# Performance work log

Measured on AMD Instinct MI355X. Metric: run time of the kernel, lower is better.

## Reference

```python
import jax, jax.numpy as jnp
import numpy as np

SCALE = 2.0 / 0.24  # UniformBoxWarp(sidelength=0.24)

def pos_embed(x, max_logscale, n_freqs):
    freqs = 2.0 ** jnp.linspace(0.0, float(max_logscale), n_freqs).astype(x.dtype)
    xb = x[..., None, :] * freqs[:, None]                  # (b, n, F, 3)
    sc = jnp.stack([jnp.sin(xb), jnp.cos(xb)], axis=-2)    # (b, n, F, 2, 3)
    sc = sc.reshape(x.shape[:-1] + (n_freqs * 2 * 3,))
    return jnp.concatenate([x, sc], axis=-1)

def film(x, W, b, freq, phase):
    # x: (b, n, in); freq/phase: (b, out) broadcast over points
    h = jnp.einsum('bni,oi->bno', x, W) + b
    return jnp.sin(freq[:, None, :] * h + phase[:, None, :])

def split_style(style):
    # rearrange 'b (2 d) -> b d 2'; freq = first half * 15 + 30, phase = second half
    d = style.shape[-1] // 2
    return style[:, :d] * 15.0 + 30.0, style[:, d:]

def setup_inputs() -> dict:
    key = jax.random.key(0)
    ks = jax.random.split(key, 14)
    B, N, H = 4, 65536, 256
    dim_pos, dim_dir = 63, 27
    r = lambda k, shp, s=1.0: jax.random.normal(k, shp, dtype=jnp.float32) * s
    return {
        'input': r(ks[0], (B, N, 3)),
        'ray_directions': r(ks[1], (B, N, 3)),
        'style_network': r(ks[2], (B, 4 * H)),
        'style_color': r(ks[3], (B, 2 * H)),
        'W1': r(ks[4], (H, dim_pos), 1.0 / dim_pos),
        'b1': jnp.zeros((H,), jnp.float32),
        'W2': r(ks[5], (H, H), np.sqrt(6.0 / H) / 25.0),
        'b2': jnp.zeros((H,), jnp.float32),
        'Wf': r(ks[6], (1, H), np.sqrt(6.0 / H) / 25.0),
        'bf': jnp.zeros((1,), jnp.float32),
        'Wcs': r(ks[7], (H, H + dim_dir), np.sqrt(6.0 / (H + dim_dir)) / 25.0),
        'bcs': jnp.zeros((H,), jnp.float32),
        'Wcl': r(ks[8], (3, H), np.sqrt(6.0 / H) / 25.0),
        'bcl': jnp.zeros((3,), jnp.float32),
    }

def reference(input, ray_directions, style_network, style_color,
              W1, b1, W2, b2, Wf, bf, Wcs, bcs, Wcl, bcl):
    H = W1.shape[0]
    pe = pos_embed(input * SCALE, 9, 10)                 # (b, n, 63)
    fn, pn = split_style(style_network)                  # (b, 2H) each
    x = film(pe, W1, b1, fn[:, :H], pn[:, :H])
    x = film(x, W2, b2, fn[:, H:], pn[:, H:])
    sigma = jnp.einsum('bnh,oh->bno', x, Wf) + bf        # (b, n, 1)
    de = pos_embed(ray_directions, 3, 4)                 # (b, n, 27)
    fc, pc = split_style(style_color)
    hc = film(jnp.concatenate([de, x], axis=-1), Wcs, bcs, fc, pc)
    rgb = jnp.einsum('bnh,oh->bno', hc, Wcl) + bcl       # (b, n, 3)
    return jnp.concatenate([rgb, sigma], axis=-1)        # (b, n, 4)
```

## Files before the change

kernel.cpp:

```cpp
#include <hip/hip_runtime.h>


#define SCALE_F 8.333333333333334f

typedef _Float16 hf;
typedef __attribute__((ext_vector_type(8)))  _Float16 hf8;
typedef __attribute__((ext_vector_type(16))) float f32x16;

__device__ __forceinline__ float redrev(float x) {
  const float chi = 0.15915494309189535f;
  const float clo = 6.4206383e-09f;
  float n = rintf(x * chi);
  float d = __builtin_fmaf(x, chi, -n);
  return __builtin_fmaf(x, clo, d);
}
__device__ __forceinline__ float fsin(float x) { return __builtin_amdgcn_sinf(redrev(x)); }
__device__ __forceinline__ float fcos(float x) { return __builtin_amdgcn_cosf(redrev(x)); }
__device__ __forceinline__ float sinrev(float t) { return __builtin_amdgcn_sinf(t - rintf(t)); }

#define INV2PI 0.15915494309189535f
#define C15R   2.3873241463784303f
#define C30R   4.7746482927568605f

__device__ __forceinline__ unsigned pk2h(hf a, hf b) {
  return ((unsigned)__builtin_bit_cast(unsigned short, a)) |
         (((unsigned)__builtin_bit_cast(unsigned short, b)) << 16);
}

__global__ void prep_w(const float* __restrict__ W1, const float* __restrict__ W2,
                       const float* __restrict__ Wcs, unsigned short* __restrict__ wsu)
{
  int t = blockIdx.x * 256 + threadIdx.x;
  if (t >= 155648) return;
  int L, pos, base;
  if (t < 16384)      { L = 0; pos = t;         base = 0; }
  else if (t < 81920) { L = 1; pos = t - 16384; base = 32768; }
  else                { L = 2; pos = t - 81920; base = 163840; }
  int kstep = pos >> 12, r = pos & 4095;
  int ot = (r >> 9) & 7, kh = (r >> 8) & 1, o5 = (r >> 3) & 31, j = r & 7;
  int o = ot * 32 + o5, k = kstep * 16 + kh * 8 + j;
  float wv = 0.f;
  if (L == 0)      { if (k < 63) wv = W1[o * 63 + k]; }
  else if (L == 1) { wv = W2[o * 256 + k]; }
  else { if (k < 256) wv = Wcs[o * 283 + 27 + k];
         else { int q = k - 256; if (q < 27) wv = Wcs[o * 283 + q]; } }
  hf hh = (hf)wv;
  hf ll = (hf)((wv - (float)hh) * 1024.0f);
  wsu[base + kstep * 8192 + r]        = __builtin_bit_cast(unsigned short, hh);
  wsu[base + kstep * 8192 + 4096 + r] = __builtin_bit_cast(unsigned short, ll);
}

__device__ __forceinline__ float peval(float x0, float x1, float x2, int k) {
  if (k >= 63) return 0.f;
  if (k < 3) return (k == 0) ? x0 : ((k == 1) ? x1 : x2);
  int rr = k - 3, f = rr / 6, rem = rr - f * 6;
  int d = (rem < 3) ? rem : rem - 3;
  float xa = (d == 0) ? x0 : ((d == 1) ? x1 : x2);
  float arg = xa * (float)(1 << f);
  return (rem < 3) ? fsin(arg) : fcos(arg);
}
__device__ __forceinline__ float deval(float r0, float r1, float r2, int k) {
  if (k >= 27) return 0.f;
  if (k < 3) return (k == 0) ? r0 : ((k == 1) ? r1 : r2);
  int rr = k - 3, f = rr / 6, rem = rr - f * 6;
  int d = (rem < 3) ? rem : rem - 3;
  float ra = (d == 0) ? r0 : ((d == 1) ? r1 : r2);
  float arg = ra * (float)(1 << f);
  return (rem < 3) ? fsin(arg) : fcos(arg);
}
__device__ __forceinline__ void build_de(float r0, float r1, float r2, int kbase,
                                         hf8& hh, hf8& ll) {
  unsigned uh[4], ul[4];
  #pragma unroll
  for (int jj = 0; jj < 4; ++jj) {
    float va = deval(r0, r1, r2, kbase + 2 * jj), vb = deval(r0, r1, r2, kbase + 2 * jj + 1);
    hf ha = (hf)va, hb = (hf)vb;
    uh[jj] = pk2h(ha, hb);
    ul[jj] = pk2h((hf)((va - (float)ha) * 1024.f), (hf)((vb - (float)hb) * 1024.f));
  }
  uint4 vh = make_uint4(uh[0], uh[1], uh[2], uh[3]);
  uint4 vl = make_uint4(ul[0], ul[1], ul[2], ul[3]);
  hh = __builtin_bit_cast(hf8, vh);
  ll = __builtin_bit_cast(hf8, vl);
}

__device__ __forceinline__ void stage_slab(const unsigned short* __restrict__ prep, int ks,
                                           unsigned short* lWb, int wv, int lane) {
  const char* src = (const char*)prep + (size_t)ks * 16384 + wv * 2048 + lane * 16;
  char* dst = (char*)lWb + wv * 2048;
  __builtin_amdgcn_global_load_lds((const unsigned int*)src, (unsigned int*)dst, 16, 0, 0);
  __builtin_amdgcn_global_load_lds((const unsigned int*)(src + 1024),
                                   (unsigned int*)(dst + 1024), 16, 0, 0);
}

__device__ __forceinline__ void kstep_mfma(const unsigned short* lwb, int wbA,
                                           hf8 Bh0, hf8 Bh1, hf8 Bl0, hf8 Bl1,
                                           f32x16& a00, f32x16& a01,
                                           f32x16& a10, f32x16& a11) {
  const hf sc = (hf)0.0009765625f;
  hf8 Bh0s = Bh0 * sc, Bh1s = Bh1 * sc, Bl0s = Bl0 * sc, Bl1s = Bl1 * sc;
  hf8 Ah0 = *(const hf8*)&lwb[wbA];
  hf8 Al0 = *(const hf8*)&lwb[4096 + wbA];
  hf8 Ah1 = *(const hf8*)&lwb[wbA + 512];
  hf8 Al1 = *(const hf8*)&lwb[4096 + wbA + 512];
  a00 = __builtin_amdgcn_mfma_f32_32x32x16_f16(Ah0, Bh0,  a00, 0, 0, 0);
  a00 = __builtin_amdgcn_mfma_f32_32x32x16_f16(Al0, Bh0s, a00, 0, 0, 0);
  a00 = __builtin_amdgcn_mfma_f32_32x32x16_f16(Ah0, Bl0s, a00, 0, 0, 0);
  a01 = __builtin_amdgcn_mfma_f32_32x32x16_f16(Ah0, Bh1,  a01, 0, 0, 0);
  a01 = __builtin_amdgcn_mfma_f32_32x32x16_f16(Al0, Bh1s, a01, 0, 0, 0);
  a01 = __builtin_amdgcn_mfma_f32_32x32x16_f16(Ah0, Bl1s, a01, 0, 0, 0);
  a10 = __builtin_amdgcn_mfma_f32_32x32x16_f16(Ah1, Bh0,  a10, 0, 0, 0);
  a10 = __builtin_amdgcn_mfma_f32_32x32x16_f16(Al1, Bh0s, a10, 0, 0, 0);
  a10 = __builtin_amdgcn_mfma_f32_32x32x16_f16(Ah1, Bl0s, a10, 0, 0, 0);
  a11 = __builtin_amdgcn_mfma_f32_32x32x16_f16(Ah1, Bh1,  a11, 0, 0, 0);
  a11 = __builtin_amdgcn_mfma_f32_32x32x16_f16(Al1, Bh1s, a11, 0, 0, 0);
  a11 = __builtin_amdgcn_mfma_f32_32x32x16_f16(Ah1, Bl1s, a11, 0, 0, 0);
}

template <int NKTOT, int NLX>
__device__ __forceinline__ void layer_loop(
    const unsigned short* __restrict__ prep, unsigned short* lW,
    const unsigned short* lX, int ptA, int ptB, int h, int wbA, int wv, int lane,
    f32x16& a00, f32x16& a01, f32x16& a10, f32x16& a11,
    hf8 dhA0, hf8 dhB0, hf8 dhA1, hf8 dhB1,
    hf8 dlA0, hf8 dlB0, hf8 dlA1, hf8 dlB1)
{
  stage_slab(prep, 0, lW, wv, lane);
  if (NKTOT > 1) stage_slab(prep, 1, lW + 8192, wv, lane);
  const int bA = ptA * 256, bB = ptB * 256, sA = ptA & 7, sB = ptB & 7;
  #pragma unroll 1
  for (int ks = 0; ks < NLX; ++ks) {
    if (ks + 1 < NKTOT) asm volatile("s_waitcnt vmcnt(2)" ::: "memory");
    else                asm volatile("s_waitcnt vmcnt(0)" ::: "memory");
    __syncthreads();
    int slot = ks * 2 + h;
    hf8 Bh0 = *(const hf8*)&lX[bA + ((slot ^ sA) << 3)];
    hf8 Bh1 = *(const hf8*)&lX[bB + ((slot ^ sB) << 3)];
    hf8 Bl0 = *(const hf8*)&lX[32768 + bA + ((slot ^ sA) << 3)];
    hf8 Bl1 = *(const hf8*)&lX[32768 + bB + ((slot ^ sB) << 3)];
    kstep_mfma(lW + (ks & 1) * 8192, wbA, Bh0, Bh1, Bl0, Bl1, a00, a01, a10, a11);
    __syncthreads();
    if (ks + 2 < NKTOT) stage_slab(prep, ks + 2, lW + (ks & 1) * 8192, wv, lane);
  }
  if (NLX < NKTOT) {
    asm volatile("s_waitcnt vmcnt(2)" ::: "memory");
    __syncthreads();
    kstep_mfma(lW + (NLX & 1) * 8192, wbA, dhA0, dhB0, dlA0, dlB0, a00, a01, a10, a11);
    __syncthreads();
    asm volatile("s_waitcnt vmcnt(0)" ::: "memory");
    __syncthreads();
    kstep_mfma(lW + ((NLX + 1) & 1) * 8192, wbA, dhA1, dhB1, dlA1, dlB1, a00, a01, a10, a11);
    __syncthreads();
  }
}

__device__ __forceinline__ void store_pair(unsigned short* lX, int pt, int slot, int off,
                                           float v0, float v1, float v2, float v3)
{
  hf h0 = (hf)v0, h1 = (hf)v1, h2 = (hf)v2, h3 = (hf)v3;
  int base = pt * 256 + ((slot ^ (pt & 7)) << 3) + off;
  *(uint2*)&lX[base] = make_uint2(pk2h(h0, h1), pk2h(h2, h3));
  hf r0 = (hf)((v0 - (float)h0) * 1024.f), r1 = (hf)((v1 - (float)h1) * 1024.f);
  hf r2 = (hf)((v2 - (float)h2) * 1024.f), r3 = (hf)((v3 - (float)h3) * 1024.f);
  *(uint2*)&lX[32768 + base] = make_uint2(pk2h(r0, r1), pk2h(r2, r3));
}

__global__ void __launch_bounds__(512, 1)
siren_mfma(const float* __restrict__ input, const float* __restrict__ rdir,
           const float* __restrict__ sn, const float* __restrict__ sc,
           const float* __restrict__ b1, const float* __restrict__ b2,
           const float* __restrict__ Wf, const float* __restrict__ bfp,
           const float* __restrict__ bcs, const float* __restrict__ Wcl,
           const float* __restrict__ bcl, const unsigned short* __restrict__ wsu,
           float* __restrict__ out)
{
  __shared__ __align__(16) unsigned char smem[163840];
  unsigned short* lX = (unsigned short*)smem;
  unsigned short* lW = (unsigned short*)(smem + 131072);
  float* lP = (float*)smem;

  const int tid = threadIdx.x;
  const int w = tid >> 6, lane = tid & 63;
  const int ow = w >> 1, pw = w & 1;
  const int l31 = lane & 31, h = lane >> 5;
  const int gpt0 = blockIdx.x << 7;
  const int b = blockIdx.x >> 9;
  const int ptA = pw * 64 + l31, ptB = ptA + 32;
  const int wbA = ow * 1024 + h * 256 + l31 * 8;
  const float* snb = sn + b * 1024;
  const float* scb = sc + b * 512;

  float rA0, rA1, rA2, rB0, rB1, rB2;
  {
    const float* rp = rdir + (size_t)(gpt0 + ptA) * 3;
    rA0 = rp[0]; rA1 = rp[1]; rA2 = rp[2];
    const float* rq = rdir + (size_t)(gpt0 + ptB) * 3;
    rB0 = rq[0]; rB1 = rq[1]; rB2 = rq[2];
  }

  {
    const int ept = tid & 127, eseg = tid >> 7;
    const float* ip = input + (size_t)(gpt0 + ept) * 3;
    float x0 = ip[0] * SCALE_F, x1 = ip[1] * SCALE_F, x2 = ip[2] * SCALE_F;
    #pragma unroll
    for (int j = 0; j < 4; ++j) {
      int k0 = eseg * 16 + 4 * j;
      float v0 = peval(x0, x1, x2, k0),     v1 = peval(x0, x1, x2, k0 + 1);
      float v2 = peval(x0, x1, x2, k0 + 2), v3 = peval(x0, x1, x2, k0 + 3);
      int slot = eseg * 2 + (j >> 1);
      store_pair(lX, ept, slot, (j & 1) * 4, v0, v1, v2, v3);
    }
  }

  f32x16 a00, a01, a10, a11;
  hf8 hz = {};
  float sp0 = 0.f, sp1 = 0.f;

  #pragma unroll
  for (int oi = 0; oi < 2; ++oi)
    #pragma unroll
    for (int q = 0; q < 4; ++q) {
      int o0 = ow * 64 + oi * 32 + q * 8 + h * 4;
      float4 bv = *(const float4*)&b1[o0];
      f32x16& aA = oi ? a10 : a00; f32x16& aB = oi ? a11 : a01;
      aA[q*4+0] = bv.x; aA[q*4+1] = bv.y; aA[q*4+2] = bv.z; aA[q*4+3] = bv.w;
      aB[q*4+0] = bv.x; aB[q*4+1] = bv.y; aB[q*4+2] = bv.z; aB[q*4+3] = bv.w;
    }
  layer_loop<4, 4>(wsu, lW, lX, ptA, ptB, h, wbA, w, lane, a00, a01, a10, a11,
                   hz, hz, hz, hz, hz, hz, hz, hz);
  #pragma unroll
  for (int oi = 0; oi < 2; ++oi)
    #pragma unroll
    for (int q = 0; q < 4; ++q) {
      int o0 = ow * 64 + oi * 32 + q * 8 + h * 4;
      float4 f4 = *(const float4*)&snb[o0];
      float4 p4 = *(const float4*)&snb[512 + o0];
      float fr0 = __builtin_fmaf(f4.x, C15R, C30R), fr1 = __builtin_fmaf(f4.y, C15R, C30R);
      float fr2 = __builtin_fmaf(f4.z, C15R, C30R), fr3 = __builtin_fmaf(f4.w, C15R, C30R);
      float pr0 = p4.x * INV2PI, pr1 = p4.y * INV2PI, pr2 = p4.z * INV2PI, pr3 = p4.w * INV2PI;
      int slot = ow * 8 + oi * 4 + q;
      #pragma unroll
      for (int pi = 0; pi < 2; ++pi) {
        const f32x16& a = pi ? (oi ? a11 : a01) : (oi ? a10 : a00);
        float v0 = sinrev(__builtin_fmaf(fr0, a[q*4+0], pr0));
        float v1 = sinrev(__builtin_fmaf(fr1, a[q*4+1], pr1));
        float v2 = sinrev(__builtin_fmaf(fr2, a[q*4+2], pr2));
        float v3 = sinrev(__builtin_fmaf(fr3, a[q*4+3], pr3));
        store_pair(lX, pi ? ptB : ptA, slot, h * 4, v0, v1, v2, v3);
      }
    }

  #pragma unroll
  for (int oi = 0; oi < 2; ++oi)
    #pragma unroll
    for (int q = 0; q < 4; ++q) {
      int o0 = ow * 64 + oi * 32 + q * 8 + h * 4;
      float4 bv = *(const float4*)&b2[o0];
      f32x16& aA = oi ? a10 : a00; f32x16& aB = oi ? a11 : a01;
      aA[q*4+0] = bv.x; aA[q*4+1] = bv.y; aA[q*4+2] = bv.z; aA[q*4+3] = bv.w;
      aB[q*4+0] = bv.x; aB[q*4+1] = bv.y; aB[q*4+2] = bv.z; aB[q*4+3] = bv.w;
    }
  layer_loop<16, 16>(wsu + 32768, lW, lX, ptA, ptB, h, wbA, w, lane, a00, a01, a10, a11,
                     hz, hz, hz, hz, hz, hz, hz, hz);
  #pragma unroll
  for (int oi = 0; oi < 2; ++oi)
    #pragma unroll
    for (int q = 0; q < 4; ++q) {
      int o0 = ow * 64 + oi * 32 + q * 8 + h * 4;
      float4 f4 = *(const float4*)&snb[256 + o0];
      float4 p4 = *(const float4*)&snb[768 + o0];
      float4 wf = *(const float4*)&Wf[o0];
      float fr0 = __builtin_fmaf(f4.x, C15R, C30R), fr1 = __builtin_fmaf(f4.y, C15R, C30R);
      float fr2 = __builtin_fmaf(f4.z, C15R, C30R), fr3 = __builtin_fmaf(f4.w, C15R, C30R);
      float pr0 = p4.x * INV2PI, pr1 = p4.y * INV2PI, pr2 = p4.z * INV2PI, pr3 = p4.w * INV2PI;
      int slot = ow * 8 + oi * 4 + q;
      #pragma unroll
      for (int pi = 0; pi < 2; ++pi) {
        const f32x16& a = pi ? (oi ? a11 : a01) : (oi ? a10 : a00);
        float v0 = sinrev(__builtin_fmaf(fr0, a[q*4+0], pr0));
        float v1 = sinrev(__builtin_fmaf(fr1, a[q*4+1], pr1));
        float v2 = sinrev(__builtin_fmaf(fr2, a[q*4+2], pr2));
        float v3 = sinrev(__builtin_fmaf(fr3, a[q*4+3], pr3));
        float s = __builtin_fmaf(wf.x, v0, __builtin_fmaf(wf.y, v1,
                  __builtin_fmaf(wf.z, v2, wf.w * v3)));
        if (pi == 0) sp0 += s; else sp1 += s;
        store_pair(lX, pi ? ptB : ptA, slot, h * 4, v0, v1, v2, v3);
      }
    }

  hf8 dhA0, dhB0, dhA1, dhB1, dlA0, dlB0, dlA1, dlB1;
  build_de(rA0, rA1, rA2, 0 * 16 + h * 8, dhA0, dlA0);
  build_de(rB0, rB1, rB2, 0 * 16 + h * 8, dhB0, dlB0);
  build_de(rA0, rA1, rA2, 1 * 16 + h * 8, dhA1, dlA1);
  build_de(rB0, rB1, rB2, 1 * 16 + h * 8, dhB1, dlB1);

  #pragma unroll
  for (int oi = 0; oi < 2; ++oi)
    #pragma unroll
    for (int q = 0; q < 4; ++q) {
      int o0 = ow * 64 + oi * 32 + q * 8 + h * 4;
      float4 bv = *(const float4*)&bcs[o0];
      f32x16& aA = oi ? a10 : a00; f32x16& aB = oi ? a11 : a01;
      aA[q*4+0] = bv.x; aA[q*4+1] = bv.y; aA[q*4+2] = bv.z; aA[q*4+3] = bv.w;
      aB[q*4+0] = bv.x; aB[q*4+1] = bv.y; aB[q*4+2] = bv.z; aB[q*4+3] = bv.w;
    }
  layer_loop<18, 16>(wsu + 163840, lW, lX, ptA, ptB, h, wbA, w, lane, a00, a01, a10, a11,
                     dhA0, dhB0, dhA1, dhB1, dlA0, dlB0, dlA1, dlB1);
  float q00 = 0.f, q01 = 0.f, q02 = 0.f, q10 = 0.f, q11 = 0.f, q12 = 0.f;
  #pragma unroll
  for (int oi = 0; oi < 2; ++oi)
    #pragma unroll
    for (int q = 0; q < 4; ++q) {
      int o0 = ow * 64 + oi * 32 + q * 8 + h * 4;
      float4 f4 = *(const float4*)&scb[o0];
      float4 p4 = *(const float4*)&scb[256 + o0];
      float4 w0 = *(const float4*)&Wcl[o0];
      float4 w1 = *(const float4*)&Wcl[256 + o0];
      float4 w2 = *(const float4*)&Wcl[512 + o0];
      float fr0 = __builtin_fmaf(f4.x, C15R, C30R), fr1 = __builtin_fmaf(f4.y, C15R, C30R);
      float fr2 = __builtin_fmaf(f4.z, C15R, C30R), fr3 = __builtin_fmaf(f4.w, C15R, C30R);
      float pr0 = p4.x * INV2PI, pr1 = p4.y * INV2PI, pr2 = p4.z * INV2PI, pr3 = p4.w * INV2PI;
      #pragma unroll
      for (int pi = 0; pi < 2; ++pi) {
        const f32x16& a = pi ? (oi ? a11 : a01) : (oi ? a10 : a00);
        float v0 = sinrev(__builtin_fmaf(fr0, a[q*4+0], pr0));
        float v1 = sinrev(__builtin_fmaf(fr1, a[q*4+1], pr1));
        float v2 = sinrev(__builtin_fmaf(fr2, a[q*4+2], pr2));
        float v3 = sinrev(__builtin_fmaf(fr3, a[q*4+3], pr3));
        float t0 = __builtin_fmaf(w0.x, v0, __builtin_fmaf(w0.y, v1, __builtin_fmaf(w0.z, v2, w0.w * v3)));
        float t1 = __builtin_fmaf(w1.x, v0, __builtin_fmaf(w1.y, v1, __builtin_fmaf(w1.z, v2, w1.w * v3)));
        float t2 = __builtin_fmaf(w2.x, v0, __builtin_fmaf(w2.y, v1, __builtin_fmaf(w2.z, v2, w2.w * v3)));
        if (pi == 0) { q00 += t0; q01 += t1; q02 += t2; }
        else         { q10 += t0; q11 += t1; q12 += t2; }
      }
    }

  q00 += __shfl_xor(q00, 32); q01 += __shfl_xor(q01, 32); q02 += __shfl_xor(q02, 32);
  q10 += __shfl_xor(q10, 32); q11 += __shfl_xor(q11, 32); q12 += __shfl_xor(q12, 32);
  sp0 += __shfl_xor(sp0, 32); sp1 += __shfl_xor(sp1, 32);
  if (h == 0) {
    *(float4*)&lP[((w * 2 + 0) * 32 + l31) * 4] = make_float4(q00, q01, q02, sp0);
    *(float4*)&lP[((w * 2 + 1) * 32 + l31) * 4] = make_float4(q10, q11, q12, sp1);
  }
  __syncthreads();

  {
    int ptL = tid >> 2, ch = tid & 3;
    int pwt = ptL >> 6, pit = (ptL >> 5) & 1, lt = ptL & 31;
    float v = 0.f;
    #pragma unroll
    for (int owt = 0; owt < 4; ++owt) {
      int wv_ = (owt * 2 + pwt);
      v += lP[((wv_ * 2 + pit) * 32 + lt) * 4 + ch];
    }
    v += (ch == 3) ? bfp[0] : bcl[ch];
    out[((size_t)gpt0 + ptL) * 4 + ch] = v;
  }
}

extern "C" void kernel_launch(void* const* d_in, const int* in_sizes, int n_in,
                              void* d_out, int out_size, void* d_ws, size_t ws_size,
                              hipStream_t stream) {
  const float* input = (const float*)d_in[0];
  const float* rdir  = (const float*)d_in[1];
  const float* sn    = (const float*)d_in[2];
  const float* sc    = (const float*)d_in[3];
  const float* W1    = (const float*)d_in[4];
  const float* b1    = (const float*)d_in[5];
  const float* W2    = (const float*)d_in[6];
  const float* b2    = (const float*)d_in[7];
  const float* Wf    = (const float*)d_in[8];
  const float* bf    = (const float*)d_in[9];
  const float* Wcs   = (const float*)d_in[10];
  const float* bcs   = (const float*)d_in[11];
  const float* Wcl   = (const float*)d_in[12];
  const float* bcl   = (const float*)d_in[13];
  unsigned short* wsu = (unsigned short*)d_ws;
  float* out = (float*)d_out;

  prep_w<<<608, 256, 0, stream>>>(W1, W2, Wcs, wsu);
  siren_mfma<<<2048, 512, 0, stream>>>(input, rdir, sn, sc, b1, b2, Wf, bf,
                                       bcs, Wcl, bcl, wsu, out);
}
```

Baseline: 320.8 us.

## Halve points per block, store activation residuals as FP8 to shrink LDS

Each block now handles 64 points instead of 128 and keeps one pair of accumulators per wave. The low-order residual of the split-fp16 activations is stored in LDS as scaled FP8 rather than fp16, which cuts shared memory from 160KB to 80KB and allows more resident blocks (launch bounds raised to 4). Weight slab staging is issued early, before the epilogue math of the previous layer, so it overlaps with that work. The cost is extra FP8 decode per k-step, the same weight slab traffic spread over twice as many points, and a less accurate residual term.

```diff
diff --git a/kernel.cpp b/kernel.cpp
--- a/kernel.cpp
+++ b/kernel.cpp
@@ -4,6 +4,8 @@
 #define SCALE_F 8.333333333333334f
 
 typedef _Float16 hf;
+typedef __attribute__((ext_vector_type(2)))  float f32x2;
+typedef __attribute__((ext_vector_type(2)))  _Float16 hf2;
 typedef __attribute__((ext_vector_type(8)))  _Float16 hf8;
 typedef __attribute__((ext_vector_type(16))) float f32x16;
 
@@ -25,6 +27,25 @@
 __device__ __forceinline__ unsigned pk2h(hf a, hf b) {
   return ((unsigned)__builtin_bit_cast(unsigned short, a)) |
          (((unsigned)__builtin_bit_cast(unsigned short, b)) << 16);
+}
+__device__ __forceinline__ unsigned enc4_fp8(float r0, float r1, float r2, float r3) {
+  int e = __builtin_amdgcn_cvt_pk_fp8_f32(r0, r1, 0, false);
+  e = __builtin_amdgcn_cvt_pk_fp8_f32(r2, r3, e, true);
+  return (unsigned)e;
+}
+__device__ __forceinline__ hf8 dec8_fp8(uint2 enc) {
+  const float dsc = 0.015625f;
+  f32x2 f0 = __builtin_amdgcn_cvt_pk_f32_fp8((int)enc.x, false);
+  f32x2 f1 = __builtin_amdgcn_cvt_pk_f32_fp8((int)enc.x, true);
+  f32x2 f2 = __builtin_amdgcn_cvt_pk_f32_fp8((int)enc.y, false);
+  f32x2 f3 = __builtin_amdgcn_cvt_pk_f32_fp8((int)enc.y, true);
+  hf2 h0 = __builtin_bit_cast(hf2, __builtin_amdgcn_cvt_pkrtz(f0.x * dsc, f0.y * dsc));
+  hf2 h1 = __builtin_bit_cast(hf2, __builtin_amdgcn_cvt_pkrtz(f1.x * dsc, f1.y * dsc));
+  hf2 h2 = __builtin_bit_cast(hf2, __builtin_amdgcn_cvt_pkrtz(f2.x * dsc, f2.y * dsc));
+  hf2 h3 = __builtin_bit_cast(hf2, __builtin_amdgcn_cvt_pkrtz(f3.x * dsc, f3.y * dsc));
+  uint4 u = make_uint4(__builtin_bit_cast(unsigned, h0), __builtin_bit_cast(unsigned, h1),
+                       __builtin_bit_cast(unsigned, h2), __builtin_bit_cast(unsigned, h3));
+  return __builtin_bit_cast(hf8, u);
 }
 
 __global__ void prep_w(const float* __restrict__ W1, const float* __restrict__ W2,
@@ -76,7 +97,7 @@
     float va = deval(r0, r1, r2, kbase + 2 * jj), vb = deval(r0, r1, r2, kbase + 2 * jj + 1);
     hf ha = (hf)va, hb = (hf)vb;
     uh[jj] = pk2h(ha, hb);
-    ul[jj] = pk2h((hf)((va - (float)ha) * 1024.f), (hf)((vb - (float)hb) * 1024.f));
+    ul[jj] = pk2h((hf)(va - (float)ha), (hf)(vb - (float)hb));
   }
   uint4 vh = make_uint4(uh[0], uh[1], uh[2], uh[3]);
   uint4 vl = make_uint4(ul[0], ul[1], ul[2], ul[3]);
@@ -92,80 +113,75 @@
   __builtin_amdgcn_global_load_lds((const unsigned int*)(src + 1024),
                                    (unsigned int*)(dst + 1024), 16, 0, 0);
 }
+__device__ __forceinline__ void stage2(const unsigned short* __restrict__ prep,
+                                       unsigned short* lW, int wv, int lane) {
+  stage_slab(prep, 0, lW, wv, lane);
+  stage_slab(prep, 1, lW + 8192, wv, lane);
+}
 
 __device__ __forceinline__ void kstep_mfma(const unsigned short* lwb, int wbA,
-                                           hf8 Bh0, hf8 Bh1, hf8 Bl0, hf8 Bl1,
-                                           f32x16& a00, f32x16& a01,
-                                           f32x16& a10, f32x16& a11) {
+                                           hf8 Bh, hf8 Blv, f32x16& a0, f32x16& a1) {
   const hf sc = (hf)0.0009765625f;
-  hf8 Bh0s = Bh0 * sc, Bh1s = Bh1 * sc, Bl0s = Bl0 * sc, Bl1s = Bl1 * sc;
+  hf8 Bhs = Bh * sc;
   hf8 Ah0 = *(const hf8*)&lwb[wbA];
   hf8 Al0 = *(const hf8*)&lwb[4096 + wbA];
   hf8 Ah1 = *(const hf8*)&lwb[wbA + 512];
   hf8 Al1 = *(const hf8*)&lwb[4096 + wbA + 512];
-  a00 = __builtin_amdgcn_mfma_f32_32x32x16_f16(Ah0, Bh0,  a00, 0, 0, 0);
-  a00 = __builtin_amdgcn_mfma_f32_32x32x16_f16(Al0, Bh0s, a00, 0, 0, 0);
-  a00 = __builtin_amdgcn_mfma_f32_32x32x16_f16(Ah0, Bl0s, a00, 0, 0, 0);
-  a01 = __builtin_amdgcn_mfma_f32_32x32x16_f16(Ah0, Bh1,  a01, 0, 0, 0);
-  a01 = __builtin_amdgcn_mfma_f32_32x32x16_f16(Al0, Bh1s, a01, 0, 0, 0);
-  a01 = __builtin_amdgcn_mfma_f32_32x32x16_f16(Ah0, Bl1s, a01, 0, 0, 0);
-  a10 = __builtin_amdgcn_mfma_f32_32x32x16_f16(Ah1, Bh0,  a10, 0, 0, 0);
-  a10 = __builtin_amdgcn_mfma_f32_32x32x16_f16(Al1, Bh0s, a10, 0, 0, 0);
-  a10 = __builtin_amdgcn_mfma_f32_32x32x16_f16(Ah1, Bl0s, a10, 0, 0, 0);
-  a11 = __builtin_amdgcn_mfma_f32_32x32x16_f16(Ah1, Bh1,  a11, 0, 0, 0);
-  a11 = __builtin_amdgcn_mfma_f32_32x32x16_f16(Al1, Bh1s, a11, 0, 0, 0);
-  a11 = __builtin_amdgcn_mfma_f32_32x32x16_f16(Ah1, Bl1s, a11, 0, 0, 0);
-}
-
-template <int NKTOT, int NLX>
+  a0 = __builtin_amdgcn_mfma_f32_32x32x16_f16(Ah0, Bh,  a0, 0, 0, 0);
+  a0 = __builtin_amdgcn_mfma_f32_32x32x16_f16(Al0, Bhs, a0, 0, 0, 0);
+  a0 = __builtin_amdgcn_mfma_f32_32x32x16_f16(Ah0, Blv, a0, 0, 0, 0);
+  a1 = __builtin_amdgcn_mfma_f32_32x32x16_f16(Ah1, Bh,  a1, 0, 0, 0);
+  a1 = __builtin_amdgcn_mfma_f32_32x32x16_f16(Al1, Bhs, a1, 0, 0, 0);
+  a1 = __builtin_amdgcn_mfma_f32_32x32x16_f16(Ah1, Blv, a1, 0, 0, 0);
+}
+
+template <int NK, bool DE>
 __device__ __forceinline__ void layer_loop(
     const unsigned short* __restrict__ prep, unsigned short* lW,
-    const unsigned short* lX, int ptA, int ptB, int h, int wbA, int wv, int lane,
-    f32x16& a00, f32x16& a01, f32x16& a10, f32x16& a11,
-    hf8 dhA0, hf8 dhB0, hf8 dhA1, hf8 dhB1,
-    hf8 dlA0, hf8 dlB0, hf8 dlA1, hf8 dlB1)
+    const unsigned short* lXh, const unsigned char* lXl,
+    int pt, int h, int wbA, int wv, int lane,
+    f32x16& a0, f32x16& a1, hf8 dh0, hf8 dh1, hf8 dl0, hf8 dl1)
 {
-  stage_slab(prep, 0, lW, wv, lane);
-  if (NKTOT > 1) stage_slab(prep, 1, lW + 8192, wv, lane);
-  const int bA = ptA * 256, bB = ptB * 256, sA = ptA & 7, sB = ptB & 7;
+  const int NLX = DE ? NK - 2 : NK;
+  const int bh = pt * 256, p7 = pt & 7, p15 = pt & 15;
   #pragma unroll 1
   for (int ks = 0; ks < NLX; ++ks) {
-    if (ks + 1 < NKTOT) asm volatile("s_waitcnt vmcnt(2)" ::: "memory");
-    else                asm volatile("s_waitcnt vmcnt(0)" ::: "memory");
+    if (ks + 1 < NK) asm volatile("s_waitcnt vmcnt(2)" ::: "memory");
+    else             asm volatile("s_waitcnt vmcnt(0)" ::: "memory");
     __syncthreads();
     int slot = ks * 2 + h;
-    hf8 Bh0 = *(const hf8*)&lX[bA + ((slot ^ sA) << 3)];
-    hf8 Bh1 = *(const hf8*)&lX[bB + ((slot ^ sB) << 3)];
-    hf8 Bl0 = *(const hf8*)&lX[32768 + bA + ((slot ^ sA) << 3)];
-    hf8 Bl1 = *(const hf8*)&lX[32768 + bB + ((slot ^ sB) << 3)];
-    kstep_mfma(lW + (ks & 1) * 8192, wbA, Bh0, Bh1, Bl0, Bl1, a00, a01, a10, a11);
-    __syncthreads();
-    if (ks + 2 < NKTOT) stage_slab(prep, ks + 2, lW + (ks & 1) * 8192, wv, lane);
-  }
-  if (NLX < NKTOT) {
+    hf8 Bh = *(const hf8*)&lXh[bh + ((slot ^ p7) << 3)];
+    uint2 enc = *(const uint2*)&lXl[bh + ((slot ^ p15) << 3)];
+    hf8 Blv = dec8_fp8(enc);
+    kstep_mfma(lW + (ks & 1) * 8192, wbA, Bh, Blv, a0, a1);
+    __syncthreads();
+    if (ks + 2 < NK) stage_slab(prep, ks + 2, lW + (ks & 1) * 8192, wv, lane);
+  }
+  if (DE) {
     asm volatile("s_waitcnt vmcnt(2)" ::: "memory");
     __syncthreads();
-    kstep_mfma(lW + (NLX & 1) * 8192, wbA, dhA0, dhB0, dlA0, dlB0, a00, a01, a10, a11);
+    kstep_mfma(lW + (NLX & 1) * 8192, wbA, dh0, dl0, a0, a1);
     __syncthreads();
     asm volatile("s_waitcnt vmcnt(0)" ::: "memory");
     __syncthreads();
-    kstep_mfma(lW + ((NLX + 1) & 1) * 8192, wbA, dhA1, dhB1, dlA1, dlB1, a00, a01, a10, a11);
-    __syncthreads();
-  }
-}
-
-__device__ __forceinline__ void store_pair(unsigned short* lX, int pt, int slot, int off,
-                                           float v0, float v1, float v2, float v3)
+    kstep_mfma(lW + ((NLX + 1) & 1) * 8192, wbA, dh1, dl1, a0, a1);
+    __syncthreads();
+  }
+}
+
+__device__ __forceinline__ void store4(unsigned short* lXh, unsigned char* lXl,
+                                       int pt, int slot, int h,
+                                       float v0, float v1, float v2, float v3)
 {
   hf h0 = (hf)v0, h1 = (hf)v1, h2 = (hf)v2, h3 = (hf)v3;
-  int base = pt * 256 + ((slot ^ (pt & 7)) << 3) + off;
-  *(uint2*)&lX[base] = make_uint2(pk2h(h0, h1), pk2h(h2, h3));
-  hf r0 = (hf)((v0 - (float)h0) * 1024.f), r1 = (hf)((v1 - (float)h1) * 1024.f);
-  hf r2 = (hf)((v2 - (float)h2) * 1024.f), r3 = (hf)((v3 - (float)h3) * 1024.f);
-  *(uint2*)&lX[32768 + base] = make_uint2(pk2h(r0, r1), pk2h(r2, r3));
-}
-
-__global__ void __launch_bounds__(512, 1)
+  *(uint2*)&lXh[pt * 256 + ((slot ^ (pt & 7)) << 3) + h * 4] =
+      make_uint2(pk2h(h0, h1), pk2h(h2, h3));
+  *(unsigned*)&lXl[pt * 256 + ((slot ^ (pt & 15)) << 3) + h * 4] =
+      enc4_fp8((v0 - (float)h0) * 64.f, (v1 - (float)h1) * 64.f,
+               (v2 - (float)h2) * 64.f, (v3 - (float)h3) * 64.f);
+}
+
+__global__ void __launch_bounds__(512, 4)
 siren_mfma(const float* __restrict__ input, const float* __restrict__ rdir,
            const float* __restrict__ sn, const float* __restrict__ sc,
            const float* __restrict__ b1, const float* __restrict__ b2,
@@ -174,47 +190,52 @@
            const float* __restrict__ bcl, const unsigned short* __restrict__ wsu,
            float* __restrict__ out)
 {
-  __shared__ __align__(16) unsigned char smem[163840];
-  unsigned short* lX = (unsigned short*)smem;
-  unsigned short* lW = (unsigned short*)(smem + 131072);
+  __shared__ __align__(16) unsigned char smem[81920];
+  unsigned short* lXh = (unsigned short*)smem;
+  unsigned char*  lXl = smem + 32768;
+  unsigned short* lW  = (unsigned short*)(smem + 49152);
   float* lP = (float*)smem;
 
   const int tid = threadIdx.x;
   const int w = tid >> 6, lane = tid & 63;
   const int ow = w >> 1, pw = w & 1;
   const int l31 = lane & 31, h = lane >> 5;
-  const int gpt0 = blockIdx.x << 7;
-  const int b = blockIdx.x >> 9;
-  const int ptA = pw * 64 + l31, ptB = ptA + 32;
+  const int gpt0 = blockIdx.x << 6;
+  const int b = blockIdx.x >> 10;
+  const int pt = pw * 32 + l31;
   const int wbA = ow * 1024 + h * 256 + l31 * 8;
   const float* snb = sn + b * 1024;
   const float* scb = sc + b * 512;
 
-  float rA0, rA1, rA2, rB0, rB1, rB2;
+  stage2(wsu, lW, w, lane);
+
+  float rA0, rA1, rA2;
   {
-    const float* rp = rdir + (size_t)(gpt0 + ptA) * 3;
+    const float* rp = rdir + (size_t)(gpt0 + pt) * 3;
     rA0 = rp[0]; rA1 = rp[1]; rA2 = rp[2];
-    const float* rq = rdir + (size_t)(gpt0 + ptB) * 3;
-    rB0 = rq[0]; rB1 = rq[1]; rB2 = rq[2];
   }
 
   {
-    const int ept = tid & 127, eseg = tid >> 7;
+    const int ept = tid & 63, seg = tid >> 6;
     const float* ip = input + (size_t)(gpt0 + ept) * 3;
     float x0 = ip[0] * SCALE_F, x1 = ip[1] * SCALE_F, x2 = ip[2] * SCALE_F;
-    #pragma unroll
-    for (int j = 0; j < 4; ++j) {
-      int k0 = eseg * 16 + 4 * j;
-      float v0 = peval(x0, x1, x2, k0),     v1 = peval(x0, x1, x2, k0 + 1);
-      float v2 = peval(x0, x1, x2, k0 + 2), v3 = peval(x0, x1, x2, k0 + 3);
-      int slot = eseg * 2 + (j >> 1);
-      store_pair(lX, ept, slot, (j & 1) * 4, v0, v1, v2, v3);
-    }
-  }
-
-  f32x16 a00, a01, a10, a11;
+    float vv[8];
+    #pragma unroll
+    for (int jj = 0; jj < 8; ++jj) vv[jj] = peval(x0, x1, x2, seg * 8 + jj);
+    hf c0=(hf)vv[0], c1=(hf)vv[1], c2=(hf)vv[2], c3=(hf)vv[3];
+    hf c4=(hf)vv[4], c5=(hf)vv[5], c6=(hf)vv[6], c7=(hf)vv[7];
+    *(uint4*)&lXh[ept * 256 + ((seg ^ (ept & 7)) << 3)] =
+        make_uint4(pk2h(c0,c1), pk2h(c2,c3), pk2h(c4,c5), pk2h(c6,c7));
+    *(uint2*)&lXl[ept * 256 + ((seg ^ (ept & 15)) << 3)] = make_uint2(
+        enc4_fp8((vv[0]-(float)c0)*64.f, (vv[1]-(float)c1)*64.f,
+                 (vv[2]-(float)c2)*64.f, (vv[3]-(float)c3)*64.f),
+        enc4_fp8((vv[4]-(float)c4)*64.f, (vv[5]-(float)c5)*64.f,
+                 (vv[6]-(float)c6)*64.f, (vv[7]-(float)c7)*64.f));
+  }
+
+  f32x16 a0, a1;
   hf8 hz = {};
-  float sp0 = 0.f, sp1 = 0.f;
+  float sp = 0.f;
 
   #pragma unroll
   for (int oi = 0; oi < 2; ++oi)
@@ -222,12 +243,11 @@
     for (int q = 0; q < 4; ++q) {
       int o0 = ow * 64 + oi * 32 + q * 8 + h * 4;
       float4 bv = *(const float4*)&b1[o0];
-      f32x16& aA = oi ? a10 : a00; f32x16& aB = oi ? a11 : a01;
-      aA[q*4+0] = bv.x; aA[q*4+1] = bv.y; aA[q*4+2] = bv.z; aA[q*4+3] = bv.w;
-      aB[q*4+0] = bv.x; aB[q*4+1] = bv.y; aB[q*4+2] = bv.z; aB[q*4+3] = bv.w;
-    }
-  layer_loop<4, 4>(wsu, lW, lX, ptA, ptB, h, wbA, w, lane, a00, a01, a10, a11,
-                   hz, hz, hz, hz, hz, hz, hz, hz);
+      f32x16& a = oi ? a1 : a0;
+      a[q*4+0] = bv.x; a[q*4+1] = bv.y; a[q*4+2] = bv.z; a[q*4+3] = bv.w;
+    }
+  layer_loop<4, false>(wsu, lW, lXh, lXl, pt, h, wbA, w, lane, a0, a1, hz, hz, hz, hz);
+  stage2(wsu + 32768, lW, w, lane);
   #pragma unroll
   for (int oi = 0; oi < 2; ++oi)
     #pragma unroll
@@ -235,19 +255,12 @@
       int o0 = ow * 64 + oi * 32 + q * 8 + h * 4;
       float4 f4 = *(const float4*)&snb[o0];
       float4 p4 = *(const float4*)&snb[512 + o0];
-      float fr0 = __builtin_fmaf(f4.x, C15R, C30R), fr1 = __builtin_fmaf(f4.y, C15R, C30R);
-      float fr2 = __builtin_fmaf(f4.z, C15R, C30R), fr3 = __builtin_fmaf(f4.w, C15R, C30R);
-      float pr0 = p4.x * INV2PI, pr1 = p4.y * INV2PI, pr2 = p4.z * INV2PI, pr3 = p4.w * INV2PI;
-      int slot = ow * 8 + oi * 4 + q;
-      #pragma unroll
-      for (int pi = 0; pi < 2; ++pi) {
-        const f32x16& a = pi ? (oi ? a11 : a01) : (oi ? a10 : a00);
-        float v0 = sinrev(__builtin_fmaf(fr0, a[q*4+0], pr0));
-        float v1 = sinrev(__builtin_fmaf(fr1, a[q*4+1], pr1));
-        float v2 = sinrev(__builtin_fmaf(fr2, a[q*4+2], pr2));
-        float v3 = sinrev(__builtin_fmaf(fr3, a[q*4+3], pr3));
-        store_pair(lX, pi ? ptB : ptA, slot, h * 4, v0, v1, v2, v3);
-      }
+      const f32x16& a = oi ? a1 : a0;
+      float v0 = sinrev(__builtin_fmaf(__builtin_fmaf(f4.x, C15R, C30R), a[q*4+0], p4.x * INV2PI));
+      float v1 = sinrev(__builtin_fmaf(__builtin_fmaf(f4.y, C15R, C30R), a[q*4+1], p4.y * INV2PI));
+      float v2 = sinrev(__builtin_fmaf(__builtin_fmaf(f4.z, C15R, C30R), a[q*4+2], p4.z * INV2PI));
+      float v3 = sinrev(__builtin_fmaf(__builtin_fmaf(f4.w, C15R, C30R), a[q*4+3], p4.w * INV2PI));
+      store4(lXh, lXl, pt, ow * 8 + oi * 4 + q, h, v0, v1, v2, v3);
     }
 
   #pragma unroll
@@ -256,12 +269,11 @@
     for (int q = 0; q < 4; ++q) {
       int o0 = ow * 64 + oi * 32 + q * 8 + h * 4;
       float4 bv = *(const float4*)&b2[o0];
-      f32x16& aA = oi ? a10 : a00; f32x16& aB = oi ? a11 : a01;
-      aA[q*4+0] = bv.x; aA[q*4+1] = bv.y; aA[q*4+2] = bv.z; aA[q*4+3] = bv.w;
-      aB[q*4+0] = bv.x; aB[q*4+1] = bv.y; aB[q*4+2] = bv.z; aB[q*4+3] = bv.w;
-    }
-  layer_loop<16, 16>(wsu + 32768, lW, lX, ptA, ptB, h, wbA, w, lane, a00, a01, a10, a11,
-                     hz, hz, hz, hz, hz, hz, hz, hz);
+      f32x16& a = oi ? a1 : a0;
+      a[q*4+0] = bv.x; a[q*4+1] = bv.y; a[q*4+2] = bv.z; a[q*4+3] = bv.w;
+    }
+  layer_loop<16, false>(wsu + 32768, lW, lXh, lXl, pt, h, wbA, w, lane, a0, a1, hz, hz, hz, hz);
+  stage2(wsu + 163840, lW, w, lane);
   #pragma unroll
   for (int oi = 0; oi < 2; ++oi)
     #pragma unroll
@@ -270,29 +282,19 @@
       float4 f4 = *(const float4*)&snb[256 + o0];
       float4 p4 = *(const float4*)&snb[768 + o0];
       float4 wf = *(const float4*)&Wf[o0];
-      float fr0 = __builtin_fmaf(f4.x, C15R, C30R), fr1 = __builtin_fmaf(f4.y, C15R, C30R);
-      float fr2 = __builtin_fmaf(f4.z, C15R, C30R), fr3 = __builtin_fmaf(f4.w, C15R, C30R);
-      float pr0 = p4.x * INV2PI, pr1 = p4.y * INV2PI, pr2 = p4.z * INV2PI, pr3 = p4.w * INV2PI;
-      int slot = ow * 8 + oi * 4 + q;
-      #pragma unroll
-      for (int pi = 0; pi < 2; ++pi) {
-        const f32x16& a = pi ? (oi ? a11 : a01) : (oi ? a10 : a00);
-        float v0 = sinrev(__builtin_fmaf(fr0, a[q*4+0], pr0));
-        float v1 = sinrev(__builtin_fmaf(fr1, a[q*4+1], pr1));
-        float v2 = sinrev(__builtin_fmaf(fr2, a[q*4+2], pr2));
-        float v3 = sinrev(__builtin_fmaf(fr3, a[q*4+3], pr3));
-        float s = __builtin_fmaf(wf.x, v0, __builtin_fmaf(wf.y, v1,
-                  __builtin_fmaf(wf.z, v2, wf.w * v3)));
-        if (pi == 0) sp0 += s; else sp1 += s;
-        store_pair(lX, pi ? ptB : ptA, slot, h * 4, v0, v1, v2, v3);
-      }
-    }
-
-  hf8 dhA0, dhB0, dhA1, dhB1, dlA0, dlB0, dlA1, dlB1;
-  build_de(rA0, rA1, rA2, 0 * 16 + h * 8, dhA0, dlA0);
-  build_de(rB0, rB1, rB2, 0 * 16 + h * 8, dhB0, dlB0);
-  build_de(rA0, rA1, rA2, 1 * 16 + h * 8, dhA1, dlA1);
-  build_de(rB0, rB1, rB2, 1 * 16 + h * 8, dhB1, dlB1);
+      const f32x16& a = oi ? a1 : a0;
+      float v0 = sinrev(__builtin_fmaf(__builtin_fmaf(f4.x, C15R, C30R), a[q*4+0], p4.x * INV2PI));
+      float v1 = sinrev(__builtin_fmaf(__builtin_fmaf(f4.y, C15R, C30R), a[q*4+1], p4.y * INV2PI));
+      float v2 = sinrev(__builtin_fmaf(__builtin_fmaf(f4.z, C15R, C30R), a[q*4+2], p4.z * INV2PI));
+      float v3 = sinrev(__builtin_fmaf(__builtin_fmaf(f4.w, C15R, C30R), a[q*4+3], p4.w * INV2PI));
+      sp = __builtin_fmaf(wf.x, v0, __builtin_fmaf(wf.y, v1,
+           __builtin_fmaf(wf.z, v2, __builtin_fmaf(wf.w, v3, sp))));
+      store4(lXh, lXl, pt, ow * 8 + oi * 4 + q, h, v0, v1, v2, v3);
+    }
+
+  hf8 dh0, dh1, dl0, dl1;
+  build_de(rA0, rA1, rA2, 0 * 16 + h * 8, dh0, dl0);
+  build_de(rA0, rA1, rA2, 1 * 16 + h * 8, dh1, dl1);
 
   #pragma unroll
   for (int oi = 0; oi < 2; ++oi)
@@ -300,13 +302,12 @@
     for (int q = 0; q < 4; ++q) {
       int o0 = ow * 64 + oi * 32 + q * 8 + h * 4;
       float4 bv = *(const float4*)&bcs[o0];
-      f32x16& aA = oi ? a10 : a00; f32x16& aB = oi ? a11 : a01;
-      aA[q*4+0] = bv.x; aA[q*4+1] = bv.y; aA[q*4+2] = bv.z; aA[q*4+3] = bv.w;
-      aB[q*4+0] = bv.x; aB[q*4+1] = bv.y; aB[q*4+2] = bv.z; aB[q*4+3] = bv.w;
-    }
-  layer_loop<18, 16>(wsu + 163840, lW, lX, ptA, ptB, h, wbA, w, lane, a00, a01, a10, a11,
-                     dhA0, dhB0, dhA1, dhB1, dlA0, dlB0, dlA1, dlB1);
-  float q00 = 0.f, q01 = 0.f, q02 = 0.f, q10 = 0.f, q11 = 0.f, q12 = 0.f;
+      f32x16& a = oi ? a1 : a0;
+      a[q*4+0] = bv.x; a[q*4+1] = bv.y; a[q*4+2] = bv.z; a[q*4+3] = bv.w;
+    }
+  layer_loop<18, true>(wsu + 163840, lW, lXh, lXl, pt, h, wbA, w, lane, a0, a1,
+                       dh0, dh1, dl0, dl1);
+  float q0 = 0.f, q1 = 0.f, q2 = 0.f;
   #pragma unroll
   for (int oi = 0; oi < 2; ++oi)
     #pragma unroll
@@ -317,42 +318,29 @@
       float4 w0 = *(const float4*)&Wcl[o0];
       float4 w1 = *(const float4*)&Wcl[256 + o0];
       float4 w2 = *(const float4*)&Wcl[512 + o0];
-      float fr0 = __builtin_fmaf(f4.x, C15R, C30R), fr1 = __builtin_fmaf(f4.y, C15R, C30R);
-      float fr2 = __builtin_fmaf(f4.z, C15R, C30R), fr3 = __builtin_fmaf(f4.w, C15R, C30R);
-      float pr0 = p4.x * INV2PI, pr1 = p4.y * INV2PI, pr2 = p4.z * INV2PI, pr3 = p4.w * INV2PI;
-      #pragma unroll
-      for (int pi = 0; pi < 2; ++pi) {
-        const f32x16& a = pi ? (oi ? a11 : a01) : (oi ? a10 : a00);
-        float v0 = sinrev(__builtin_fmaf(fr0, a[q*4+0], pr0));
-        float v1 = sinrev(__builtin_fmaf(fr1, a[q*4+1], pr1));
-        float v2 = sinrev(__builtin_fmaf(fr2, a[q*4+2], pr2));
-        float v3 = sinrev(__builtin_fmaf(fr3, a[q*4+3], pr3));
-        float t0 = __builtin_fmaf(w0.x, v0, __builtin_fmaf(w0.y, v1, __builtin_fmaf(w0.z, v2, w0.w * v3)));
-        float t1 = __builtin_fmaf(w1.x, v0, __builtin_fmaf(w1.y, v1, __builtin_fmaf(w1.z, v2, w1.w * v3)));
-        float t2 = __builtin_fmaf(w2.x, v0, __builtin_fmaf(w2.y, v1, __builtin_fmaf(w2.z, v2, w2.w * v3)));
-        if (pi == 0) { q00 += t0; q01 += t1; q02 += t2; }
-        else         { q10 += t0; q11 += t1; q12 += t2; }
-      }
-    }
-
-  q00 += __shfl_xor(q00, 32); q01 += __shfl_xor(q01, 32); q02 += __shfl_xor(q02, 32);
-  q10 += __shfl_xor(q10, 32); q11 += __shfl_xor(q11, 32); q12 += __shfl_xor(q12, 32);
-  sp0 += __shfl_xor(sp0, 32); sp1 += __shfl_xor(sp1, 32);
-  if (h == 0) {
-    *(float4*)&lP[((w * 2 + 0) * 32 + l31) * 4] = make_float4(q00, q01, q02, sp0);
-    *(float4*)&lP[((w * 2 + 1) * 32 + l31) * 4] = make_float4(q10, q11, q12, sp1);
-  }
+      const f32x16& a = oi ? a1 : a0;
+      float v0 = sinrev(__builtin_fmaf(__builtin_fmaf(f4.x, C15R, C30R), a[q*4+0], p4.x * INV2PI));
+      float v1 = sinrev(__builtin_fmaf(__builtin_fmaf(f4.y, C15R, C30R), a[q*4+1], p4.y * INV2PI));
+      float v2 = sinrev(__builtin_fmaf(__builtin_fmaf(f4.z, C15R, C30R), a[q*4+2], p4.z * INV2PI));
+      float v3 = sinrev(__builtin_fmaf(__builtin_fmaf(f4.w, C15R, C30R), a[q*4+3], p4.w * INV2PI));
+      q0 = __builtin_fmaf(w0.x, v0, __builtin_fmaf(w0.y, v1, __builtin_fmaf(w0.z, v2, __builtin_fmaf(w0.w, v3, q0))));
+      q1 = __builtin_fmaf(w1.x, v0, __builtin_fmaf(w1.y, v1, __builtin_fmaf(w1.z, v2, __builtin_fmaf(w1.w, v3, q1))));
+      q2 = __builtin_fmaf(w2.x, v0, __builtin_fmaf(w2.y, v1, __builtin_fmaf(w2.z, v2, __builtin_fmaf(w2.w, v3, q2))));
+    }
+
+  q0 += __shfl_xor(q0, 32); q1 += __shfl_xor(q1, 32); q2 += __shfl_xor(q2, 32);
+  sp += __shfl_xor(sp, 32);
+  if (h == 0)
+    *(float4*)&lP[(w * 32 + l31) * 4] = make_float4(q0, q1, q2, sp);
   __syncthreads();
 
-  {
+  if (tid < 256) {
     int ptL = tid >> 2, ch = tid & 3;
-    int pwt = ptL >> 6, pit = (ptL >> 5) & 1, lt = ptL & 31;
+    int pwt = ptL >> 5, lt = ptL & 31;
     float v = 0.f;
     #pragma unroll
-    for (int owt = 0; owt < 4; ++owt) {
-      int wv_ = (owt * 2 + pwt);
-      v += lP[((wv_ * 2 + pit) * 32 + lt) * 4 + ch];
-    }
+    for (int owt = 0; owt < 4; ++owt)
+      v += lP[((owt * 2 + pwt) * 32 + lt) * 4 + ch];
     v += (ch == 3) ? bfp[0] : bcl[ch];
     out[((size_t)gpt0 + ptL) * 4 + ch] = v;
   }
@@ -379,6 +367,6 @@
   float* out = (float*)d_out;
 
   prep_w<<<608, 256, 0, stream>>>(W1, W2, Wcs, wsu);
-  siren_mfma<<<2048, 512, 0, stream>>>(input, rdir, sn, sc, b1, b2, Wf, bf,
+  siren_mfma<<<4096, 512, 0, stream>>>(input, rdir, sn, sc, b1, b2, Wf, bf,
                                        bcs, Wcl, bcl, wsu, out);
 }
```

Result: slower. 342.7 us (+6.8%).
